# Optimization experiments

Hardware: AMD Instinct MI355X
Metric: run time of the kernel (lower is better)

Reference implementation:

```python
import jax, jax.numpy as jnp
import numpy as np
from jax import lax

B, T, IN, H = 256, 128, 512, 1024
C = IN + H  # concat size


def setup_inputs() -> dict:
    key = jax.random.key(0)
    ks = jax.random.split(key, 32)
    d = {}
    names = ["F", "O", "CY", "CI", "CP", "CN", "IY", "II", "IP", "IN"]
    for i, n in enumerate(names):
        d["W" + n] = jax.random.normal(ks[i], (C, H), jnp.float32) * (2.0 / C) ** 0.5
        d["b" + n] = jax.random.uniform(ks[10 + i], (H,), jnp.float32)
    d["wA"] = jax.random.normal(ks[20], (H, H), jnp.float32) * (2.0 / H) ** 0.5
    for j, n in enumerate(["bAY", "bAI", "bAP", "bAN"]):
        d[n] = jax.random.uniform(ks[21 + j], (H,), jnp.float32)
    for j, n in enumerate(["factorY", "factorI", "factorP", "factorN"]):
        d[n] = jax.random.normal(ks[25 + j], (B, T, IN), jnp.float32)
    return d


def reference(factorY, factorI, factorP, factorN,
              WF, bF, WO, bO, WCY, bCY, WCI, bCI, WCP, bCP, WCN, bCN,
              WIY, bIY, WII, bII, WIP, bIP, WIN, bIN,
              wA, bAY, bAI, bAP, bAN):
    Bq = factorY.shape[0]
    Hq = WF.shape[1]

    def step(carry, xs):
        cT, hT = carry
        yT, iT, pT, nT = xs
        hy = jnp.concatenate([hT, yT], -1)  # [B, C]
        hi = jnp.concatenate([hT, iT], -1)
        hp = jnp.concatenate([hT, pT], -1)
        hn = jnp.concatenate([hT, nT], -1)
        f = jax.nn.sigmoid(hy @ WF + bF)
        o = jax.nn.sigmoid(hy @ WO + bO)
        # candidate memories gated by input gates (all input gates use hTyT, per source)
        lY = jnp.tanh(hy @ WCY + bCY) * jax.nn.sigmoid(hy @ WIY + bIY)
        lI = jnp.tanh(hi @ WCI + bCI) * jax.nn.sigmoid(hy @ WII + bII)
        lP = jnp.tanh(hp @ WCP + bCP) * jax.nn.sigmoid(hy @ WIP + bIP)
        lN = jnp.tanh(hn @ WCN + bCN) * jax.nn.sigmoid(hy @ WIN + bIN)
        cwa = cT @ wA  # [B, H]
        # faithful quirk: [B,1] score + [H] bias broadcasts to [B,H]; softmax over 4H
        att = jnp.concatenate([
            jnp.tanh(jnp.sum(lY * cwa, -1, keepdims=True) + bAY),
            jnp.tanh(jnp.sum(lI * cwa, -1, keepdims=True) + bAI),
            jnp.tanh(jnp.sum(lP * cwa, -1, keepdims=True) + bAP),
            jnp.tanh(jnp.sum(lN * cwa, -1, keepdims=True) + bAN)], -1)  # [B, 4H]
        a = jax.nn.softmax(att, -1)
        lT = a[:, 0:1] * lY + a[:, 1:2] * lI + a[:, 2:3] * lP + a[:, 3:4] * lN
        cN = cT * f + lT
        hN = jnp.tanh(cN) * o
        return (cN, hN), hN

    xs = (jnp.swapaxes(factorY, 0, 1), jnp.swapaxes(factorI, 0, 1),
          jnp.swapaxes(factorP, 0, 1), jnp.swapaxes(factorN, 0, 1))
    z = jnp.zeros((Bq, Hq), factorY.dtype)
    _, hs = lax.scan(step, (z, z), xs)  # hs: [T, B, H]
    return jnp.swapaxes(hs, 0, 1)  # [B, T, H]
```

## Files before the change

kernel.cpp:

```cpp
#include <hip/hip_runtime.h>
#include <hip/hip_bf16.h>

#define H_ 1024
#define C_ 1536
#define B_ 256
#define T_ 128
#define IN_ 512
#define BH_ (B_*H_)

typedef __hip_bfloat16 bf16;
typedef __attribute__((ext_vector_type(8))) short short8;
typedef __attribute__((ext_vector_type(4))) float f32x4;
typedef unsigned int u32;

struct WPtrs { const float* W[10]; const float* wA; };
struct BPtrs { const float* b[10]; const float* bA[4]; };

__device__ __forceinline__ float sigmf(float x){ return 1.0f/(1.0f + __expf(-x)); }
__device__ __forceinline__ float tanhfast(float x){ return 1.0f - 2.0f/(__expf(2.0f*x) + 1.0f); }

__device__ __forceinline__ ushort bf16bits(float f){
    bf16 b = __float2bfloat16(f);
    return *reinterpret_cast<ushort*>(&b);
}
__device__ __forceinline__ float bf2f(ushort u){
    bf16 b = *reinterpret_cast<bf16*>(&u);
    return __bfloat162float(b);
}

__device__ __forceinline__ void gload16(const void* g, void* l){
    __builtin_amdgcn_global_load_lds((const __attribute__((address_space(1))) u32*)g,
                                     (__attribute__((address_space(3))) u32*)l, 16, 0, 0);
}

__global__ void transpose_w(WPtrs wp, ushort* __restrict__ Wt, ushort* __restrict__ wAt)
{
    int g = blockIdx.z;
    int K = (g==10) ? H_ : C_;
    int k0 = blockIdx.x*32, n0 = blockIdx.y*32;
    if (k0 >= K) return;
    const float* src = (g==10) ? wp.wA : wp.W[g];
    __shared__ float tile[32][33];
    int tx = threadIdx.x, ty = threadIdx.y;
    #pragma unroll
    for (int i=0;i<32;i+=8)
        tile[ty+i][tx] = src[(size_t)(k0+ty+i)*H_ + n0 + tx];
    __syncthreads();
    ushort* dst = (g==10) ? wAt : (Wt + (size_t)g*H_*C_);
    #pragma unroll
    for (int i=0;i<32;i+=8)
        dst[(size_t)(n0+ty+i)*K + k0 + tx] = bf16bits(tile[tx][ty+i]);
}

__global__ void convert_x(const float* __restrict__ xY, const float* __restrict__ xI,
                          const float* __restrict__ xP, const float* __restrict__ xN,
                          ushort* __restrict__ xb)
{
    size_t idx = (size_t)blockIdx.x*blockDim.x + threadIdx.x;
    size_t base = idx*4;
    size_t a = base >> 24;
    size_t off = base & ((size_t)(1u<<24)-1);
    const float* s = (a==0)?xY:(a==1)?xI:(a==2)?xP:xN;
    float4 v = *(const float4*)(s + off);
    ushort4 o;
    o.x = bf16bits(v.x); o.y = bf16bits(v.y); o.z = bf16bits(v.z); o.w = bf16bits(v.w);
    *(ushort4*)(xb + base) = o;
}

__global__ __launch_bounds__(256) void xp_gemm(const ushort* __restrict__ Wt,
                                               const ushort* __restrict__ xb,
                                               ushort* __restrict__ Xp)
{
    int bid = blockIdx.x;
    int xcd = bid & 7, lid = bid >> 3;
    int ntile = xcd*20 + (lid >> 9);
    int mtile = lid & 511;
    int g = ntile >> 4;
    int n0g = (ntile & 15)*64;
    int tq = mtile >> 2;
    int b0 = (mtile & 3)*64;
    int xs = (g==3)?1:(g==4)?2:(g==5)?3:0;
    const ushort* xsrc = xb + (size_t)xs*((size_t)B_*T_*IN_);
    const ushort* Bbase = Wt + (size_t)g*H_*C_ + 1024;

    __shared__ ushort As[64][64];
    __shared__ ushort Bs[64][64];
    int tid = threadIdx.x;
    int wid = tid>>6, lane = tid&63;
    int wr = wid>>1, wc = wid&1;

    f32x4 acc[2][2] = {};
    for (int k0=0; k0<IN_; k0+=64){
        #pragma unroll
        for (int it=0; it<2; ++it){
            int cid = it*256 + tid;
            int row = cid>>3, kc = cid&7;
            int kcs = kc ^ (row&7);
            gload16(xsrc + ((size_t)(b0+row)*T_ + tq)*IN_ + k0 + kcs*8,
                    (ushort*)As + (size_t)(it*256 + wid*64)*8);
        }
        #pragma unroll
        for (int it=0; it<2; ++it){
            int cid = it*256 + tid;
            int row = cid>>3, kc = cid&7;
            int kcs = kc ^ (row&7);
            gload16(Bbase + (size_t)(n0g+row)*C_ + k0 + kcs*8,
                    (ushort*)Bs + (size_t)(it*256 + wid*64)*8);
        }
        __syncthreads();
        #pragma unroll
        for (int kk=0; kk<2; ++kk){
            short8 af[2], bfr[2];
            #pragma unroll
            for (int mr=0;mr<2;++mr){
                int r = wr*32 + mr*16 + (lane&15);
                int j = (kk*4 + (lane>>4)) ^ (r&7);
                af[mr] = *(const short8*)((ushort*)As + r*64 + j*8);
            }
            #pragma unroll
            for (int nr=0;nr<2;++nr){
                int r = wc*32 + nr*16 + (lane&15);
                int j = (kk*4 + (lane>>4)) ^ (r&7);
                bfr[nr] = *(const short8*)((ushort*)Bs + r*64 + j*8);
            }
            #pragma unroll
            for (int mr=0;mr<2;++mr)
                #pragma unroll
                for (int nr=0;nr<2;++nr)
                    acc[mr][nr] = __builtin_amdgcn_mfma_f32_16x16x32_bf16(af[mr], bfr[nr], acc[mr][nr], 0,0,0);
        }
        __syncthreads();
    }
    ushort* Xg = Xp + (((size_t)tq*10 + g)*B_ + b0)*H_ + n0g;
    #pragma unroll
    for (int mr=0;mr<2;++mr){
        #pragma unroll
        for (int nr=0;nr<2;++nr){
            int col = wc*32 + nr*16 + (lane&15);
            #pragma unroll
            for (int r=0;r<4;++r){
                int row = wr*32 + mr*16 + (lane>>4)*4 + r;
                Xg[(size_t)row*H_ + col] = bf16bits(acc[mr][nr][r]);
            }
        }
    }
}

template<bool XP>
__global__ __launch_bounds__(128, 2) void gemm_step(
    const ushort* __restrict__ Wt, const ushort* __restrict__ wAt,
    const ushort* __restrict__ xb, const ushort* __restrict__ hb,
    const ushort* __restrict__ cbuf, const ushort* __restrict__ Xp,
    float* __restrict__ P, int t)
{
    int bid = blockIdx.x;
    int xcd = bid & 7, lid = bid >> 3;
    int ntile = xcd*11 + (lid >> 3);
    int rem = lid & 7;
    int mtile = rem >> 1;
    int split = rem & 1;
    int nglob0 = ntile*128;
    int g = nglob0 >> 10;
    int n0g = nglob0 & 1023;
    int m0 = mtile*64;
    bool isA = (g==10);
    const ushort* Bbase = isA ? wAt : (Wt + (size_t)g*H_*C_);
    size_t Bstride = isA ? 1024 : 1536;
    int kStart, kEnd;
    if (XP || isA){ kStart = split*512; kEnd = kStart + 512; }
    else          { kStart = split*768; kEnd = kStart + 768; }
    int xs = (g==3)?1:(g==4)?2:(g==5)?3:0;
    const ushort* xsrc = xb + (size_t)xs*((size_t)B_*T_*IN_);
    const ushort* Ah = isA ? cbuf : hb;

    __shared__ ushort As[2][64*64];
    __shared__ ushort Bs[2][128*64];
    int tid = threadIdx.x;
    int wid = tid>>6, lane = tid&63;

    auto stage = [&](int buf, int k0){
        ushort* la = As[buf];
        ushort* lb = Bs[buf];
        #pragma unroll
        for (int it=0; it<4; ++it){
            int cid = it*128 + tid;
            int row = cid>>3, kc = cid&7;
            int kcs = kc ^ (row&7);
            int k = k0 + kcs*8;
            const ushort* src;
            if (XP || isA || k < 1024) src = Ah + (size_t)(m0+row)*H_ + k;
            else                       src = xsrc + ((size_t)(m0+row)*T_ + t)*IN_ + (k-1024);
            gload16(src, la + (size_t)(it*128 + wid*64)*8);
        }
        #pragma unroll
        for (int it=0; it<8; ++it){
            int cid = it*128 + tid;
            int row = cid>>3, kc = cid&7;
            int kcs = kc ^ (row&7);
            gload16(Bbase + (size_t)(n0g+row)*Bstride + k0 + kcs*8,
                    lb + (size_t)(it*128 + wid*64)*8);
        }
    };

    f32x4 acc[4][4] = {};
    stage(0, kStart);

    if (XP && !isA && split==0){
        const ushort* Xg = Xp + (((size_t)t*10 + g)*B_ + m0)*H_ + n0g;
        #pragma unroll
        for (int mr=0;mr<4;++mr)
            #pragma unroll
            for (int nr=0;nr<4;++nr){
                int col = wid*64 + nr*16 + (lane&15);
                #pragma unroll
                for (int r=0;r<4;++r){
                    int row = mr*16 + (lane>>4)*4 + r;
                    acc[mr][nr][r] = bf2f(Xg[(size_t)row*H_ + col]);
                }
            }
    }
    __syncthreads();

    int nIter = (kEnd - kStart) >> 6;
    for (int i=0; i<nIter; ++i){
        int cur = i & 1;
        if (i+1 < nIter) stage(cur^1, kStart + ((i+1)<<6));
        ushort* la = As[cur];
        ushort* lb = Bs[cur];
        #pragma unroll
        for (int kk=0; kk<2; ++kk){
            short8 af[4], bfr[4];
            #pragma unroll
            for (int mr=0;mr<4;++mr){
                int r = mr*16 + (lane&15);
                int j = (kk*4 + (lane>>4)) ^ (r&7);
                af[mr] = *(const short8*)(la + r*64 + j*8);
            }
            #pragma unroll
            for (int nr=0;nr<4;++nr){
                int r = wid*64 + nr*16 + (lane&15);
                int j = (kk*4 + (lane>>4)) ^ (r&7);
                bfr[nr] = *(const short8*)(lb + r*64 + j*8);
            }
            #pragma unroll
            for (int mr=0;mr<4;++mr)
                #pragma unroll
                for (int nr=0;nr<4;++nr)
                    acc[mr][nr] = __builtin_amdgcn_mfma_f32_16x16x32_bf16(af[mr], bfr[nr], acc[mr][nr], 0,0,0);
        }
        __syncthreads();
    }

    float* Pg = P + ((size_t)split*11 + g)*BH_;
    #pragma unroll
    for (int mr=0;mr<4;++mr){
        #pragma unroll
        for (int nr=0;nr<4;++nr){
            int col = n0g + wid*64 + nr*16 + (lane&15);
            #pragma unroll
            for (int r=0;r<4;++r){
                int rowg = m0 + mr*16 + (lane>>4)*4 + r;
                Pg[(size_t)rowg*H_ + col] = acc[mr][nr][r];
            }
        }
    }
}

__global__ __launch_bounds__(1024) void step_update(
    const float* __restrict__ P, BPtrs bp,
    float* __restrict__ c, ushort* __restrict__ hb, ushort* __restrict__ cbuf,
    float* __restrict__ out, int t)
{
    int b = blockIdx.x;
    int j = threadIdx.x;
    int wid = j>>6, lane = j&63;
    const float* Pb = P + (size_t)b*H_;

    auto gp = [&](int g){
        return Pb[(size_t)g*BH_ + j] + Pb[(size_t)(11+g)*BH_ + j];
    };

    float fv = sigmf(gp(0) + bp.b[0][j]);
    float ov = sigmf(gp(1) + bp.b[1][j]);
    float lY = tanhfast(gp(2) + bp.b[2][j]) * sigmf(gp(6) + bp.b[6][j]);
    float lI = tanhfast(gp(3) + bp.b[3][j]) * sigmf(gp(7) + bp.b[7][j]);
    float lP = tanhfast(gp(4) + bp.b[4][j]) * sigmf(gp(8) + bp.b[8][j]);
    float lN = tanhfast(gp(5) + bp.b[5][j]) * sigmf(gp(9) + bp.b[9][j]);
    float cw = gp(10);

    float v0=lY*cw, v1=lI*cw, v2=lP*cw, v3=lN*cw;
    #pragma unroll
    for (int d=32; d>=1; d>>=1){
        v0 += __shfl_down(v0,d); v1 += __shfl_down(v1,d);
        v2 += __shfl_down(v2,d); v3 += __shfl_down(v3,d);
    }
    __shared__ float red[16][4];
    if (lane==0){ red[wid][0]=v0; red[wid][1]=v1; red[wid][2]=v2; red[wid][3]=v3; }
    __syncthreads();
    float sY=0, sI=0, sP=0, sN=0;
    #pragma unroll
    for (int w=0; w<16; ++w){
        sY += red[w][0]; sI += red[w][1]; sP += red[w][2]; sN += red[w][3];
    }

    float zp = __expf(tanhfast(sY + bp.bA[0][j]))
             + __expf(tanhfast(sI + bp.bA[1][j]))
             + __expf(tanhfast(sP + bp.bA[2][j]))
             + __expf(tanhfast(sN + bp.bA[3][j]));
    #pragma unroll
    for (int d=32; d>=1; d>>=1) zp += __shfl_down(zp,d);
    __shared__ float zred[16];
    if (lane==0) zred[wid] = zp;
    __syncthreads();
    float Z = 0;
    #pragma unroll
    for (int w=0; w<16; ++w) Z += zred[w];
    float Zi = 1.0f / Z;
    float a0 = __expf(tanhfast(sY + bp.bA[0][0]))*Zi;
    float a1 = __expf(tanhfast(sY + bp.bA[0][1]))*Zi;
    float a2 = __expf(tanhfast(sY + bp.bA[0][2]))*Zi;
    float a3 = __expf(tanhfast(sY + bp.bA[0][3]))*Zi;

    float lT = a0*lY + a1*lI + a2*lP + a3*lN;
    float cn = c[(size_t)b*H_ + j]*fv + lT;
    c[(size_t)b*H_ + j] = cn;
    cbuf[(size_t)b*H_ + j] = bf16bits(cn);
    float hn = tanhfast(cn)*ov;
    hb[(size_t)b*H_ + j] = bf16bits(hn);
    out[((size_t)b*T_ + t)*H_ + j] = hn;
}

extern "C" void kernel_launch(void* const* d_in, const int* in_sizes, int n_in,
                              void* d_out, int out_size, void* d_ws, size_t ws_size,
                              hipStream_t stream)
{
    WPtrs wp; BPtrs bp;
    for (int i=0;i<10;++i){ wp.W[i] = (const float*)d_in[2*i]; bp.b[i] = (const float*)d_in[2*i+1]; }
    wp.wA = (const float*)d_in[20];
    for (int i=0;i<4;++i) bp.bA[i] = (const float*)d_in[21+i];
    const float* xY = (const float*)d_in[25];
    const float* xI = (const float*)d_in[26];
    const float* xP = (const float*)d_in[27];
    const float* xN = (const float*)d_in[28];

    char* w = (char*)d_ws;
    size_t off = 0;
    ushort* Wt  = (ushort*)(w+off); off += (size_t)10*H_*C_*2;
    ushort* wAt = (ushort*)(w+off); off += (size_t)H_*H_*2;
    ushort* xb  = (ushort*)(w+off); off += (size_t)4*B_*T_*IN_*2;
    float*  P   = (float*)(w+off);  off += (size_t)22*BH_*4;
    float*  c   = (float*)(w+off);  off += (size_t)BH_*4;
    ushort* hb  = (ushort*)(w+off); off += (size_t)BH_*2;
    ushort* cbuf= (ushort*)(w+off); off += (size_t)BH_*2;
    ushort* Xp  = (ushort*)(w+off);
    size_t need_xp = off + (size_t)T_*10*B_*H_*2;
    bool xp_ok = (ws_size >= need_xp);

    hipMemsetAsync(c, 0, (size_t)BH_*8, stream);

    transpose_w<<<dim3(C_/32, H_/32, 11), dim3(32,8), 0, stream>>>(wp, Wt, wAt);
    convert_x<<<(4u*B_*T_*IN_/4)/256, 256, 0, stream>>>(xY,xI,xP,xN, xb);

    float* out = (float*)d_out;
    if (xp_ok){
        xp_gemm<<<81920, 256, 0, stream>>>(Wt, xb, Xp);
        for (int t=0;t<T_;++t){
            gemm_step<true><<<704, 128, 0, stream>>>(Wt, wAt, xb, hb, cbuf, Xp, P, t);
            step_update<<<B_, 1024, 0, stream>>>(P, bp, c, hb, cbuf, out, t);
        }
    } else {
        for (int t=0;t<T_;++t){
            gemm_step<false><<<704, 128, 0, stream>>>(Wt, wAt, xb, hb, cbuf, Xp, P, t);
            step_update<<<B_, 1024, 0, stream>>>(P, bp, c, hb, cbuf, out, t);
        }
    }
}
```

Baseline: 3.601 ms.

## Drop input precompute GEMM; read fp32 inputs directly in recurrent step GEMM

Removes the bulk convert_x and xp_gemm precompute, which materialised all input projections for every timestep in a large bf16 workspace. Each per-step GEMM now covers the full 1536-long K range, loading the fp32 input slice into registers and converting it to bf16 into LDS after the MFMA work on the current buffer. This avoids the large upfront GEMM and the reads of its output, but each recurrent step does more work (12 instead of 8 K iterations for gate tiles) on the serial critical path.

```diff
diff --git a/kernel.cpp b/kernel.cpp
--- a/kernel.cpp
+++ b/kernel.cpp
@@ -22,10 +22,6 @@
 __device__ __forceinline__ ushort bf16bits(float f){
     bf16 b = __float2bfloat16(f);
     return *reinterpret_cast<ushort*>(&b);
-}
-__device__ __forceinline__ float bf2f(ushort u){
-    bf16 b = *reinterpret_cast<bf16*>(&u);
-    return __bfloat162float(b);
 }
 
 __device__ __forceinline__ void gload16(const void* g, void* l){
@@ -52,105 +48,11 @@
         dst[(size_t)(n0+ty+i)*K + k0 + tx] = bf16bits(tile[tx][ty+i]);
 }
 
-__global__ void convert_x(const float* __restrict__ xY, const float* __restrict__ xI,
-                          const float* __restrict__ xP, const float* __restrict__ xN,
-                          ushort* __restrict__ xb)
-{
-    size_t idx = (size_t)blockIdx.x*blockDim.x + threadIdx.x;
-    size_t base = idx*4;
-    size_t a = base >> 24;
-    size_t off = base & ((size_t)(1u<<24)-1);
-    const float* s = (a==0)?xY:(a==1)?xI:(a==2)?xP:xN;
-    float4 v = *(const float4*)(s + off);
-    ushort4 o;
-    o.x = bf16bits(v.x); o.y = bf16bits(v.y); o.z = bf16bits(v.z); o.w = bf16bits(v.w);
-    *(ushort4*)(xb + base) = o;
-}
-
-__global__ __launch_bounds__(256) void xp_gemm(const ushort* __restrict__ Wt,
-                                               const ushort* __restrict__ xb,
-                                               ushort* __restrict__ Xp)
-{
-    int bid = blockIdx.x;
-    int xcd = bid & 7, lid = bid >> 3;
-    int ntile = xcd*20 + (lid >> 9);
-    int mtile = lid & 511;
-    int g = ntile >> 4;
-    int n0g = (ntile & 15)*64;
-    int tq = mtile >> 2;
-    int b0 = (mtile & 3)*64;
-    int xs = (g==3)?1:(g==4)?2:(g==5)?3:0;
-    const ushort* xsrc = xb + (size_t)xs*((size_t)B_*T_*IN_);
-    const ushort* Bbase = Wt + (size_t)g*H_*C_ + 1024;
-
-    __shared__ ushort As[64][64];
-    __shared__ ushort Bs[64][64];
-    int tid = threadIdx.x;
-    int wid = tid>>6, lane = tid&63;
-    int wr = wid>>1, wc = wid&1;
-
-    f32x4 acc[2][2] = {};
-    for (int k0=0; k0<IN_; k0+=64){
-        #pragma unroll
-        for (int it=0; it<2; ++it){
-            int cid = it*256 + tid;
-            int row = cid>>3, kc = cid&7;
-            int kcs = kc ^ (row&7);
-            gload16(xsrc + ((size_t)(b0+row)*T_ + tq)*IN_ + k0 + kcs*8,
-                    (ushort*)As + (size_t)(it*256 + wid*64)*8);
-        }
-        #pragma unroll
-        for (int it=0; it<2; ++it){
-            int cid = it*256 + tid;
-            int row = cid>>3, kc = cid&7;
-            int kcs = kc ^ (row&7);
-            gload16(Bbase + (size_t)(n0g+row)*C_ + k0 + kcs*8,
-                    (ushort*)Bs + (size_t)(it*256 + wid*64)*8);
-        }
-        __syncthreads();
-        #pragma unroll
-        for (int kk=0; kk<2; ++kk){
-            short8 af[2], bfr[2];
-            #pragma unroll
-            for (int mr=0;mr<2;++mr){
-                int r = wr*32 + mr*16 + (lane&15);
-                int j = (kk*4 + (lane>>4)) ^ (r&7);
-                af[mr] = *(const short8*)((ushort*)As + r*64 + j*8);
-            }
-            #pragma unroll
-            for (int nr=0;nr<2;++nr){
-                int r = wc*32 + nr*16 + (lane&15);
-                int j = (kk*4 + (lane>>4)) ^ (r&7);
-                bfr[nr] = *(const short8*)((ushort*)Bs + r*64 + j*8);
-            }
-            #pragma unroll
-            for (int mr=0;mr<2;++mr)
-                #pragma unroll
-                for (int nr=0;nr<2;++nr)
-                    acc[mr][nr] = __builtin_amdgcn_mfma_f32_16x16x32_bf16(af[mr], bfr[nr], acc[mr][nr], 0,0,0);
-        }
-        __syncthreads();
-    }
-    ushort* Xg = Xp + (((size_t)tq*10 + g)*B_ + b0)*H_ + n0g;
-    #pragma unroll
-    for (int mr=0;mr<2;++mr){
-        #pragma unroll
-        for (int nr=0;nr<2;++nr){
-            int col = wc*32 + nr*16 + (lane&15);
-            #pragma unroll
-            for (int r=0;r<4;++r){
-                int row = wr*32 + mr*16 + (lane>>4)*4 + r;
-                Xg[(size_t)row*H_ + col] = bf16bits(acc[mr][nr][r]);
-            }
-        }
-    }
-}
-
-template<bool XP>
 __global__ __launch_bounds__(128, 2) void gemm_step(
     const ushort* __restrict__ Wt, const ushort* __restrict__ wAt,
-    const ushort* __restrict__ xb, const ushort* __restrict__ hb,
-    const ushort* __restrict__ cbuf, const ushort* __restrict__ Xp,
+    const float* __restrict__ xY, const float* __restrict__ xI,
+    const float* __restrict__ xPf, const float* __restrict__ xNf,
+    const ushort* __restrict__ hb, const ushort* __restrict__ cbuf,
     float* __restrict__ P, int t)
 {
     int bid = blockIdx.x;
@@ -159,18 +61,15 @@
     int rem = lid & 7;
     int mtile = rem >> 1;
     int split = rem & 1;
-    int nglob0 = ntile*128;
-    int g = nglob0 >> 10;
-    int n0g = nglob0 & 1023;
+    int g = ntile >> 3;
+    int n0g = (ntile & 7)*128;
     int m0 = mtile*64;
     bool isA = (g==10);
     const ushort* Bbase = isA ? wAt : (Wt + (size_t)g*H_*C_);
     size_t Bstride = isA ? 1024 : 1536;
-    int kStart, kEnd;
-    if (XP || isA){ kStart = split*512; kEnd = kStart + 512; }
-    else          { kStart = split*768; kEnd = kStart + 768; }
-    int xs = (g==3)?1:(g==4)?2:(g==5)?3:0;
-    const ushort* xsrc = xb + (size_t)xs*((size_t)B_*T_*IN_);
+    int kStart = isA ? split*512 : split*768;
+    int nIter  = isA ? 8 : 12;
+    const float* xf = (g==3)?xI:(g==4)?xPf:(g==5)?xNf:xY;
     const ushort* Ah = isA ? cbuf : hb;
 
     __shared__ ushort As[2][64*64];
@@ -178,20 +77,10 @@
     int tid = threadIdx.x;
     int wid = tid>>6, lane = tid&63;
 
-    auto stage = [&](int buf, int k0){
-        ushort* la = As[buf];
+    float xr0[8], xr1[8], xr2[8], xr3[8];
+
+    auto stageB = [&](int buf, int k0){
         ushort* lb = Bs[buf];
-        #pragma unroll
-        for (int it=0; it<4; ++it){
-            int cid = it*128 + tid;
-            int row = cid>>3, kc = cid&7;
-            int kcs = kc ^ (row&7);
-            int k = k0 + kcs*8;
-            const ushort* src;
-            if (XP || isA || k < 1024) src = Ah + (size_t)(m0+row)*H_ + k;
-            else                       src = xsrc + ((size_t)(m0+row)*T_ + t)*IN_ + (k-1024);
-            gload16(src, la + (size_t)(it*128 + wid*64)*8);
-        }
         #pragma unroll
         for (int it=0; it<8; ++it){
             int cid = it*128 + tid;
@@ -201,30 +90,60 @@
                     lb + (size_t)(it*128 + wid*64)*8);
         }
     };
+    auto stageA_h = [&](int buf, int k0){
+        ushort* la = As[buf];
+        #pragma unroll
+        for (int it=0; it<4; ++it){
+            int cid = it*128 + tid;
+            int row = cid>>3, kc = cid&7;
+            int kcs = kc ^ (row&7);
+            gload16(Ah + (size_t)(m0+row)*H_ + k0 + kcs*8,
+                    la + (size_t)(it*128 + wid*64)*8);
+        }
+    };
+    auto stageX_issue = [&](int k0){
+        #pragma unroll
+        for (int it=0; it<4; ++it){
+            int cid = it*128 + tid;
+            int row = cid>>3, kc = cid&7;
+            const float4* s4 = (const float4*)(xf + ((size_t)(m0+row)*T_ + t)*IN_ + (k0 + kc*8 - 1024));
+            float4 a = s4[0], b = s4[1];
+            float* xr = (it==0)?xr0:(it==1)?xr1:(it==2)?xr2:xr3;
+            xr[0]=a.x; xr[1]=a.y; xr[2]=a.z; xr[3]=a.w;
+            xr[4]=b.x; xr[5]=b.y; xr[6]=b.z; xr[7]=b.w;
+        }
+    };
+    auto stageX_finish = [&](int buf){
+        ushort* la = As[buf];
+        #pragma unroll
+        for (int it=0; it<4; ++it){
+            int cid = it*128 + tid;
+            int row = cid>>3, kc = cid&7;
+            int kcs = kc ^ (row&7);
+            const float* xr = (it==0)?xr0:(it==1)?xr1:(it==2)?xr2:xr3;
+            ushort t8[8];
+            #pragma unroll
+            for (int q=0;q<8;++q) t8[q] = bf16bits(xr[q]);
+            *(ulong2*)(la + (size_t)row*64 + kcs*8) = *(ulong2*)t8;
+        }
+    };
 
     f32x4 acc[4][4] = {};
-    stage(0, kStart);
-
-    if (XP && !isA && split==0){
-        const ushort* Xg = Xp + (((size_t)t*10 + g)*B_ + m0)*H_ + n0g;
-        #pragma unroll
-        for (int mr=0;mr<4;++mr)
-            #pragma unroll
-            for (int nr=0;nr<4;++nr){
-                int col = wid*64 + nr*16 + (lane&15);
-                #pragma unroll
-                for (int r=0;r<4;++r){
-                    int row = mr*16 + (lane>>4)*4 + r;
-                    acc[mr][nr][r] = bf2f(Xg[(size_t)row*H_ + col]);
-                }
-            }
-    }
-    __syncthreads();
-
-    int nIter = (kEnd - kStart) >> 6;
+    stageA_h(0, kStart);
+    stageB(0, kStart);
+    __syncthreads();
+
+    int cur = 0;
     for (int i=0; i<nIter; ++i){
-        int cur = i & 1;
-        if (i+1 < nIter) stage(cur^1, kStart + ((i+1)<<6));
+        int k0n = kStart + ((i+1)<<6);
+        bool more = (i+1 < nIter);
+        bool nx_x = false;
+        if (more){
+            nx_x = (!isA) && (k0n >= 1024);
+            if (nx_x) stageX_issue(k0n);
+            else      stageA_h(cur^1, k0n);
+            stageB(cur^1, k0n);
+        }
         ushort* la = As[cur];
         ushort* lb = Bs[cur];
         #pragma unroll
@@ -248,7 +167,9 @@
                 for (int nr=0;nr<4;++nr)
                     acc[mr][nr] = __builtin_amdgcn_mfma_f32_16x16x32_bf16(af[mr], bfr[nr], acc[mr][nr], 0,0,0);
         }
+        if (more && nx_x) stageX_finish(cur^1);
         __syncthreads();
+        cur ^= 1;
     }
 
     float* Pg = P + ((size_t)split*11 + g)*BH_;
@@ -347,31 +268,18 @@
     size_t off = 0;
     ushort* Wt  = (ushort*)(w+off); off += (size_t)10*H_*C_*2;
     ushort* wAt = (ushort*)(w+off); off += (size_t)H_*H_*2;
-    ushort* xb  = (ushort*)(w+off); off += (size_t)4*B_*T_*IN_*2;
     float*  P   = (float*)(w+off);  off += (size_t)22*BH_*4;
     float*  c   = (float*)(w+off);  off += (size_t)BH_*4;
     ushort* hb  = (ushort*)(w+off); off += (size_t)BH_*2;
     ushort* cbuf= (ushort*)(w+off); off += (size_t)BH_*2;
-    ushort* Xp  = (ushort*)(w+off);
-    size_t need_xp = off + (size_t)T_*10*B_*H_*2;
-    bool xp_ok = (ws_size >= need_xp);
 
     hipMemsetAsync(c, 0, (size_t)BH_*8, stream);
 
     transpose_w<<<dim3(C_/32, H_/32, 11), dim3(32,8), 0, stream>>>(wp, Wt, wAt);
-    convert_x<<<(4u*B_*T_*IN_/4)/256, 256, 0, stream>>>(xY,xI,xP,xN, xb);
 
     float* out = (float*)d_out;
-    if (xp_ok){
-        xp_gemm<<<81920, 256, 0, stream>>>(Wt, xb, Xp);
-        for (int t=0;t<T_;++t){
-            gemm_step<true><<<704, 128, 0, stream>>>(Wt, wAt, xb, hb, cbuf, Xp, P, t);
-            step_update<<<B_, 1024, 0, stream>>>(P, bp, c, hb, cbuf, out, t);
-        }
-    } else {
-        for (int t=0;t<T_;++t){
-            gemm_step<false><<<704, 128, 0, stream>>>(Wt, wAt, xb, hb, cbuf, Xp, P, t);
-            step_update<<<B_, 1024, 0, stream>>>(P, bp, c, hb, cbuf, out, t);
-        }
-    }
-}
+    for (int t=0;t<T_;++t){
+        gemm_step<<<704, 128, 0, stream>>>(Wt, wAt, xY, xI, xP, xN, hb, cbuf, P, t);
+        step_update<<<B_, 1024, 0, stream>>>(P, bp, c, hb, cbuf, out, t);
+    }
+}
```

Result: slower. 3.691 ms (+2.5%).
